# Optimization experiments

Measured on AMD Instinct MI355X. Metric: run time of the kernel, lower is better.

## Reference

```python
import jax, jax.numpy as jnp
import numpy as np

R = 6                 # max displacement / padding
D = 2 * R + 1         # window side; D*D = 169 displacements


def setup_inputs() -> dict:
    key = jax.random.key(0)
    k1, k2, k3 = jax.random.split(key, 3)
    b, cf, h, w = 2, 32, 256, 256
    feats_t = jax.random.normal(k1, (b, cf, h, w), jnp.float32)
    feats_r = jax.random.normal(k2, (b, cf, h, w), jnp.float32)
    img_r = jax.random.uniform(k3, (b, 1, h, w), jnp.float32)
    return {"feats_t": feats_t, "feats_r": feats_r, "img_r": img_r}


def _forward(feats_t, feats_r, img_r):
    b, cf, h, w = feats_t.shape
    ci = img_r.shape[1]
    x2p = jnp.pad(feats_r, ((0, 0), (0, 0), (R, R), (R, R)))
    imgp = jnp.pad(img_r, ((0, 0), (0, 0), (R, R), (R, R)))
    # displacement offsets in the same order as the torch double loop (_y outer, _x inner)
    offs = jnp.stack(
        jnp.meshgrid(jnp.arange(D), jnp.arange(D), indexing="ij"), axis=-1
    ).reshape(-1, 2)

    def step(carry, off):
        dy, dx = off[0], off[1]
        win = jax.lax.dynamic_slice(x2p, (0, 0, dy, dx), (b, cf, h, w))
        c = jnp.sum(feats_t * win, axis=1)  # [b, h, w] correlation for this displacement
        iw = jax.lax.dynamic_slice(imgp, (0, 0, dy, dx), (b, ci, h, w))
        return carry, (c, iw)

    _, (corr, imgs) = jax.lax.scan(step, 0, offs)  # corr: [D*D, b, h, w]; imgs: [D*D, b, ci, h, w]
    attn = jax.nn.softmax(corr, axis=0)  # softmax over displacements (torch dim=1 channel axis)
    # weighted sum of shifted reference images -> warped target image
    return jnp.einsum("dbhw,dbchw->bchw", attn, imgs)


def reference(feats_t, feats_r, img_r):
    return _forward(feats_t, feats_r, img_r)
```

## Files before the change

### kernel.cpp

```cpp
#include <hip/hip_runtime.h>
#include <stdint.h>

typedef _Float16 half_t;
typedef _Float16 v4h __attribute__((ext_vector_type(4)));
typedef _Float16 v8h __attribute__((ext_vector_type(8)));
typedef float v4f __attribute__((ext_vector_type(4)));

#define HH 256
#define WW 256
#define HW (HH*WW)
#define TH 32
#define TW 16
#define NROWS (TH+12)
#define NPX   (TW+16)
#define PXS   40
#define NTHREADS 1024
#define NUNITS (NROWS*64)
#define L2E 1.44269504088896340736f

__global__ __launch_bounds__(NTHREADS, 4)
void corr_recon(const float* __restrict__ ft, const float* __restrict__ fr,
                const float* __restrict__ img, float* __restrict__ out)
{
    __shared__ half_t frl[NROWS * NPX * PXS];
    __shared__ float  img_lds[NROWS * NPX];

    const int bid0 = blockIdx.x;
    const int bid  = (bid0 & 7) * 32 + (bid0 >> 3);

    const int b0  = bid >> 7;
    const int rb  = bid & 127;
    const int y0  = (rb >> 4) * TH;
    const int x0t = (rb & 15) * TW;

    const int tid  = threadIdx.x;
    const int lane = tid & 63;
    const int w    = tid >> 6;
    const int n    = lane & 15;
    const int g    = lane >> 4;

    const float* frb = fr  + (size_t)b0 * 32 * HW;
    const float* ftb = ft  + (size_t)b0 * 32 * HW;
    const float* imb = img + (size_t)b0 * HW;

    auto ld_unit = [&](int i, float4* t4) {
        const int px4 = i & 7;
        const int q   = (i >> 3) & 7;
        const int row = i >> 6;
        const int gy  = y0 - 6 + row;
        const int gx  = x0t - 6 + px4 * 4;
        const int gyc = min(max(gy, 0), HH-1);
        const bool oky = (gy == gyc);
        const float* src = frb + ((size_t)(4*q) * HH + gyc) * WW;
        if (oky && gx >= 0 && gx + 3 < WW) {
            #pragma unroll
            for (int jc = 0; jc < 4; ++jc)
                t4[jc] = *(const float4*)(src + (size_t)jc * HW + gx);
        } else {
            #pragma unroll
            for (int jc = 0; jc < 4; ++jc) {
                float e0 = 0.f, e1 = 0.f, e2 = 0.f, e3 = 0.f;
                const float* s = src + (size_t)jc * HW;
                if (oky) {
                    int x0 = gx, x1 = gx+1, x2 = gx+2, x3 = gx+3;
                    e0 = (x0 >= 0 && x0 < WW) ? s[x0] : 0.f;
                    e1 = (x1 >= 0 && x1 < WW) ? s[x1] : 0.f;
                    e2 = (x2 >= 0 && x2 < WW) ? s[x2] : 0.f;
                    e3 = (x3 >= 0 && x3 < WW) ? s[x3] : 0.f;
                }
                t4[jc].x = e0; t4[jc].y = e1; t4[jc].z = e2; t4[jc].w = e3;
            }
        }
    };
    auto wr_unit = [&](int i, const float4* t4) {
        const int px4 = i & 7;
        const int q   = (i >> 3) & 7;
        const int row = i >> 6;
        const int qo  = 8*(q & 3) + 4*(q >> 2);
        const float t0[4] = {t4[0].x, t4[0].y, t4[0].z, t4[0].w};
        const float t1[4] = {t4[1].x, t4[1].y, t4[1].z, t4[1].w};
        const float t2[4] = {t4[2].x, t4[2].y, t4[2].z, t4[2].w};
        const float t3[4] = {t4[3].x, t4[3].y, t4[3].z, t4[3].w};
        #pragma unroll
        for (int jp = 0; jp < 4; ++jp) {
            const int px = px4 * 4 + jp;
            v4h pk;
            pk[0] = (half_t)t0[jp]; pk[1] = (half_t)t1[jp];
            pk[2] = (half_t)t2[jp]; pk[3] = (half_t)t3[jp];
            *(v4h*)&frl[(row * NPX + px) * PXS + qo] = pk;
        }
    };

    {
        float4 tA[4], tB[4];
        ld_unit(tid, tA);
        ld_unit(tid + NTHREADS, tB);
        wr_unit(tid, tA);
        if (tid < NUNITS - 2*NTHREADS)
            ld_unit(tid + 2*NTHREADS, tA);
        wr_unit(tid + NTHREADS, tB);
        if (tid < NUNITS - 2*NTHREADS)
            wr_unit(tid + 2*NTHREADS, tA);
    }

    if (tid < NROWS * 8) {
        const int px4 = tid & 7;
        const int row = tid >> 3;
        const int gy = y0 - 6 + row;
        const int gx = x0t - 6 + px4*4;
        const int gyc = min(max(gy, 0), HH-1);
        const bool oky = (gy == gyc);
        const float* p = imb + (size_t)gyc * WW;
        float v[4];
        if (oky && gx >= 0 && gx + 3 < WW) {
            float4 t4 = *(const float4*)(p + gx);
            v[0]=t4.x; v[1]=t4.y; v[2]=t4.z; v[3]=t4.w;
        } else {
            #pragma unroll
            for (int e = 0; e < 4; ++e) {
                int x = gx + e;
                v[e] = (oky && x >= 0 && x < WW) ? p[x] : 0.f;
            }
        }
        float4 f4; f4.x=v[0]; f4.y=v[1]; f4.z=v[2]; f4.w=v[3];
        *(float4*)&img_lds[row*NPX + px4*4] = f4;
    }

    const int y = y0 + 2*w;
    v8h a0, a1;
    {
        const float* fa = ftb + (size_t)y * WW + (x0t + n);
        #pragma unroll
        for (int j = 0; j < 4; ++j) {
            a0[j]   = (half_t)(fa[(size_t)(4*g + j)      * HW] * L2E);
            a0[4+j] = (half_t)(fa[(size_t)(16 + 4*g + j) * HW] * L2E);
            a1[j]   = (half_t)(fa[WW + (size_t)(4*g + j)      * HW] * L2E);
            a1[4+j] = (half_t)(fa[WW + (size_t)(16 + 4*g + j) * HW] * L2E);
        }
    }

    v4f bias0, bias1;
    #pragma unroll
    for (int r = 0; r < 4; ++r) {
        const int m  = 4*g + r;
        const int d0 = n - m;
        const int d1 = 16 + n - m;
        bias0[r] = (d0 >= 0 && d0 <= 12) ? 0.f : -1e4f;
        bias1[r] = (d1 >= 0 && d1 <= 12) ? 0.f : -1e4f;
    }
    const int dm = n - 4*g;

    __syncthreads();

    v4f lp0 = {0,0,0,0}, ap0 = {0,0,0,0};
    v4f lp1 = {0,0,0,0}, ap1 = {0,0,0,0};

    auto STEP = [&](const v8h& a, v4f& lp, v4f& ap,
                    const v8h& B0, const v8h& B1, float iw0, float iw1) {
        v4f c0 = __builtin_amdgcn_mfma_f32_16x16x32_f16(a, B0, bias0, 0, 0, 0);
        v4f c1 = __builtin_amdgcn_mfma_f32_16x16x32_f16(a, B1, bias1, 0, 0, 0);
        #pragma unroll
        for (int r = 0; r < 4; ++r) {
            const bool cond = (dm >= r);
            float cs  = cond ? c0[r] : c1[r];
            float iws = cond ? iw0   : iw1;
            float e = __builtin_amdgcn_exp2f(cs);
            lp[r] += e;
            ap[r] += e * iws;
        }
    };

    const half_t* prd = &frl[(2*w * NPX + n) * PXS + 8*g];
    const float*  ird = &img_lds[2*w * NPX + n];

    v8h C0 = *(const v8h*)(prd);
    v8h C1 = *(const v8h*)(prd + 16*PXS);
    float ci0 = ird[0], ci1 = ird[16];

    prd += NPX*PXS; ird += NPX;
    v8h N0 = *(const v8h*)(prd);
    v8h N1 = *(const v8h*)(prd + 16*PXS);
    float ni0 = ird[0], ni1 = ird[16];

    STEP(a0, lp0, ap0, C0, C1, ci0, ci1);

    #pragma unroll 1
    for (int rr = 1; rr < 13; ++rr) {
        C0 = N0; C1 = N1; ci0 = ni0; ci1 = ni1;
        prd += NPX*PXS; ird += NPX;
        N0 = *(const v8h*)(prd);
        N1 = *(const v8h*)(prd + 16*PXS);
        ni0 = ird[0]; ni1 = ird[16];
        STEP(a0, lp0, ap0, C0, C1, ci0, ci1);
        STEP(a1, lp1, ap1, C0, C1, ci0, ci1);
    }
    STEP(a1, lp1, ap1, N0, N1, ni0, ni1);

    #pragma unroll
    for (int r = 0; r < 4; ++r) {
        float l0 = lp0[r], v0 = ap0[r], l1 = lp1[r], v1 = ap1[r];
        l0 += __shfl_xor(l0, 1);  v0 += __shfl_xor(v0, 1);
        l1 += __shfl_xor(l1, 1);  v1 += __shfl_xor(v1, 1);
        l0 += __shfl_xor(l0, 2);  v0 += __shfl_xor(v0, 2);
        l1 += __shfl_xor(l1, 2);  v1 += __shfl_xor(v1, 2);
        l0 += __shfl_xor(l0, 4);  v0 += __shfl_xor(v0, 4);
        l1 += __shfl_xor(l1, 4);  v1 += __shfl_xor(v1, 4);
        l0 += __shfl_xor(l0, 8);  v0 += __shfl_xor(v0, 8);
        l1 += __shfl_xor(l1, 8);  v1 += __shfl_xor(v1, 8);
        lp0[r] = l0; ap0[r] = v0; lp1[r] = l1; ap1[r] = v1;
    }
    if (n < 4) {
        const float l0 = n==0 ? lp0[0] : n==1 ? lp0[1] : n==2 ? lp0[2] : lp0[3];
        const float v0 = n==0 ? ap0[0] : n==1 ? ap0[1] : n==2 ? ap0[2] : ap0[3];
        const float l1 = n==0 ? lp1[0] : n==1 ? lp1[1] : n==2 ? lp1[2] : lp1[3];
        const float v1 = n==0 ? ap1[0] : n==1 ? ap1[1] : n==2 ? ap1[2] : ap1[3];
        float* orow = out + (size_t)b0 * HW + (size_t)y * WW + x0t + 4*g + n;
        orow[0]  = v0 / l0;
        orow[WW] = v1 / l1;
    }
}

extern "C" void kernel_launch(void* const* d_in, const int* in_sizes, int n_in,
                              void* d_out, int out_size, void* d_ws, size_t ws_size,
                              hipStream_t stream)
{
    const float* ft  = (const float*)d_in[0];
    const float* fr  = (const float*)d_in[1];
    const float* img = (const float*)d_in[2];
    float* out = (float*)d_out;
    (void)in_sizes; (void)n_in; (void)out_size; (void)d_ws; (void)ws_size;
    corr_recon<<<256, NTHREADS, 0, stream>>>(ft, fr, img, out);
}
```

Baseline: 19.09 us.

## Stage LDS fill in three phases overlapped with partial per-warp compute

The single up-front fill of the shared reference-feature tile, followed by one barrier, is replaced by three phases of 16 rows each. After each phase, every warp processes as many displacement rows as are already in shared memory. Meanwhile the global loads for the next 16 rows are in flight and are written to shared memory afterwards. The aim is to hide global-load latency behind MFMA and exp work, at the cost of two extra block barriers and four extra padded rows of loads.

Result: slower. 20.97 us (+9.9%).

```diff
diff --git a/kernel.cpp b/kernel.cpp
--- a/kernel.cpp
+++ b/kernel.cpp
@@ -11,19 +11,18 @@
 #define HW (HH*WW)
 #define TH 32
 #define TW 16
-#define NROWS (TH+12)
+#define NRLDS 48
 #define NPX   (TW+16)
 #define PXS   40
 #define NTHREADS 1024
-#define NUNITS (NROWS*64)
 #define L2E 1.44269504088896340736f
 
 __global__ __launch_bounds__(NTHREADS, 4)
 void corr_recon(const float* __restrict__ ft, const float* __restrict__ fr,
                 const float* __restrict__ img, float* __restrict__ out)
 {
-    __shared__ half_t frl[NROWS * NPX * PXS];
-    __shared__ float  img_lds[NROWS * NPX];
+    __shared__ half_t frl[NRLDS * NPX * PXS];
+    __shared__ float  img_lds[NRLDS * NPX];
 
     const int bid0 = blockIdx.x;
     const int bid  = (bid0 & 7) * 32 + (bid0 >> 3);
@@ -43,7 +42,7 @@
     const float* ftb = ft  + (size_t)b0 * 32 * HW;
     const float* imb = img + (size_t)b0 * HW;
 
-    auto ld_unit = [&](int i, float4* t4) {
+    auto LD = [&](int i, float4* t4) {
         const int px4 = i & 7;
         const int q   = (i >> 3) & 7;
         const int row = i >> 6;
@@ -59,20 +58,19 @@
         } else {
             #pragma unroll
             for (int jc = 0; jc < 4; ++jc) {
-                float e0 = 0.f, e1 = 0.f, e2 = 0.f, e3 = 0.f;
                 const float* s = src + (size_t)jc * HW;
+                float e0=0.f, e1=0.f, e2=0.f, e3=0.f;
                 if (oky) {
-                    int x0 = gx, x1 = gx+1, x2 = gx+2, x3 = gx+3;
-                    e0 = (x0 >= 0 && x0 < WW) ? s[x0] : 0.f;
-                    e1 = (x1 >= 0 && x1 < WW) ? s[x1] : 0.f;
-                    e2 = (x2 >= 0 && x2 < WW) ? s[x2] : 0.f;
-                    e3 = (x3 >= 0 && x3 < WW) ? s[x3] : 0.f;
+                    e0 = (gx   >= 0 && gx   < WW) ? s[gx]   : 0.f;
+                    e1 = (gx+1 >= 0 && gx+1 < WW) ? s[gx+1] : 0.f;
+                    e2 = (gx+2 >= 0 && gx+2 < WW) ? s[gx+2] : 0.f;
+                    e3 = (gx+3 >= 0 && gx+3 < WW) ? s[gx+3] : 0.f;
                 }
-                t4[jc].x = e0; t4[jc].y = e1; t4[jc].z = e2; t4[jc].w = e3;
+                t4[jc].x=e0; t4[jc].y=e1; t4[jc].z=e2; t4[jc].w=e3;
             }
         }
     };
-    auto wr_unit = [&](int i, const float4* t4) {
+    auto WR = [&](int i, const float4* t4) {
         const int px4 = i & 7;
         const int q   = (i >> 3) & 7;
         const int row = i >> 6;
@@ -91,19 +89,10 @@
         }
     };
 
-    {
-        float4 tA[4], tB[4];
-        ld_unit(tid, tA);
-        ld_unit(tid + NTHREADS, tB);
-        wr_unit(tid, tA);
-        if (tid < NUNITS - 2*NTHREADS)
-            ld_unit(tid + 2*NTHREADS, tA);
-        wr_unit(tid + NTHREADS, tB);
-        if (tid < NUNITS - 2*NTHREADS)
-            wr_unit(tid + 2*NTHREADS, tA);
-    }
-
-    if (tid < NROWS * 8) {
+    float4 tc[4], tn[4];
+    LD(tid, tc);
+
+    if (tid < NRLDS * 8) {
         const int px4 = tid & 7;
         const int row = tid >> 3;
         const int gy = y0 - 6 + row;
@@ -139,6 +128,9 @@
         }
     }
 
+    WR(tid, tc);
+    LD(tid + NTHREADS, tn);
+
     v4f bias0, bias1;
     #pragma unroll
     for (int r = 0; r < 4; ++r) {
@@ -150,10 +142,13 @@
     }
     const int dm = n - 4*g;
 
-    __syncthreads();
-
     v4f lp0 = {0,0,0,0}, ap0 = {0,0,0,0};
     v4f lp1 = {0,0,0,0}, ap1 = {0,0,0,0};
+    const half_t* prd = &frl[(2*w * NPX + n) * PXS + 8*g];
+    const float*  ird = &img_lds[2*w * NPX + n];
+    v8h C0, C1, N0, N1;
+    float ci0 = 0.f, ci1 = 0.f, ni0 = 0.f, ni1 = 0.f;
+    int rr = 0;
 
     auto STEP = [&](const v8h& a, v4f& lp, v4f& ap,
                     const v8h& B0, const v8h& B1, float iw0, float iw1) {
@@ -170,31 +165,47 @@
         }
     };
 
-    const half_t* prd = &frl[(2*w * NPX + n) * PXS + 8*g];
-    const float*  ird = &img_lds[2*w * NPX + n];
-
-    v8h C0 = *(const v8h*)(prd);
-    v8h C1 = *(const v8h*)(prd + 16*PXS);
-    float ci0 = ird[0], ci1 = ird[16];
-
-    prd += NPX*PXS; ird += NPX;
-    v8h N0 = *(const v8h*)(prd);
-    v8h N1 = *(const v8h*)(prd + 16*PXS);
-    float ni0 = ird[0], ni1 = ird[16];
-
-    STEP(a0, lp0, ap0, C0, C1, ci0, ci1);
-
-    #pragma unroll 1
-    for (int rr = 1; rr < 13; ++rr) {
-        C0 = N0; C1 = N1; ci0 = ni0; ci1 = ni1;
-        prd += NPX*PXS; ird += NPX;
-        N0 = *(const v8h*)(prd);
-        N1 = *(const v8h*)(prd + 16*PXS);
-        ni0 = ird[0]; ni1 = ird[16];
-        STEP(a0, lp0, ap0, C0, C1, ci0, ci1);
-        STEP(a1, lp1, ap1, C0, C1, ci0, ci1);
-    }
-    STEP(a1, lp1, ap1, N0, N1, ni0, ni1);
+    auto run_until = [&](int lim) {
+        if (lim > 14) lim = 14;
+        if (rr >= lim) return;
+        if (rr == 0) {
+            C0 = *(const v8h*)(prd);  C1 = *(const v8h*)(prd + 16*PXS);
+            ci0 = ird[0]; ci1 = ird[16];
+            prd += NPX*PXS; ird += NPX;
+            N0 = *(const v8h*)(prd);  N1 = *(const v8h*)(prd + 16*PXS);
+            ni0 = ird[0]; ni1 = ird[16];
+            STEP(a0, lp0, ap0, C0, C1, ci0, ci1);
+            rr = 1;
+        }
+        const int top = (lim < 13) ? lim : 13;
+        #pragma unroll 1
+        for (; rr < top; ++rr) {
+            C0 = N0; C1 = N1; ci0 = ni0; ci1 = ni1;
+            prd += NPX*PXS; ird += NPX;
+            N0 = *(const v8h*)(prd);
+            N1 = *(const v8h*)(prd + 16*PXS);
+            ni0 = ird[0]; ni1 = ird[16];
+            STEP(a0, lp0, ap0, C0, C1, ci0, ci1);
+            STEP(a1, lp1, ap1, C0, C1, ci0, ci1);
+        }
+        if (lim == 14 && rr == 13) {
+            STEP(a1, lp1, ap1, N0, N1, ni0, ni1);
+            rr = 14;
+        }
+    };
+
+    __syncthreads();
+
+    run_until(15 - 2*w);
+    WR(tid + NTHREADS, tn);
+    LD(tid + 2*NTHREADS, tn);
+    __syncthreads();
+
+    run_until(31 - 2*w);
+    WR(tid + 2*NTHREADS, tn);
+    __syncthreads();
+
+    run_until(14);
 
     #pragma unroll
     for (int r = 0; r < 4; ++r) {
```

## Split LDS staging into two phases to overlap reference-feature loads with compute

Applied to the files above, without the earlier changes.

The reference-feature tile is now staged in two parts. The first 29 rows are written to LDS and the first half of the output rows is computed while the remaining rows are fetched from global memory. Those rows are written to LDS afterwards, behind a second barrier. Each wave now processes rows w and w+16 instead of two adjacent rows, which lets the first half depend only on the early rows. The cost is that the two row passes no longer share the B-fragment and image reads from LDS, so LDS read traffic doubles, and there is an extra barrier.

Result: slower. 21.09 us (+10.5%).

```diff
diff --git a/kernel.cpp b/kernel.cpp
--- a/kernel.cpp
+++ b/kernel.cpp
@@ -11,19 +11,20 @@
 #define HW (HH*WW)
 #define TH 32
 #define TW 16
-#define NROWS (TH+12)
+#define NRLDS 45
 #define NPX   (TW+16)
 #define PXS   40
+#define RSTEP (NPX*PXS)
 #define NTHREADS 1024
-#define NUNITS (NROWS*64)
+#define UA 1856
 #define L2E 1.44269504088896340736f
 
 __global__ __launch_bounds__(NTHREADS, 4)
 void corr_recon(const float* __restrict__ ft, const float* __restrict__ fr,
                 const float* __restrict__ img, float* __restrict__ out)
 {
-    __shared__ half_t frl[NROWS * NPX * PXS];
-    __shared__ float  img_lds[NROWS * NPX];
+    __shared__ half_t frl[NRLDS * RSTEP];
+    __shared__ float  img_lds[NRLDS * NPX];
 
     const int bid0 = blockIdx.x;
     const int bid  = (bid0 & 7) * 32 + (bid0 >> 3);
@@ -43,7 +44,7 @@
     const float* ftb = ft  + (size_t)b0 * 32 * HW;
     const float* imb = img + (size_t)b0 * HW;
 
-    auto ld_unit = [&](int i, float4* t4) {
+    auto LD = [&](int i, float4* t4) {
         const int px4 = i & 7;
         const int q   = (i >> 3) & 7;
         const int row = i >> 6;
@@ -59,20 +60,19 @@
         } else {
             #pragma unroll
             for (int jc = 0; jc < 4; ++jc) {
-                float e0 = 0.f, e1 = 0.f, e2 = 0.f, e3 = 0.f;
                 const float* s = src + (size_t)jc * HW;
+                float e0=0.f, e1=0.f, e2=0.f, e3=0.f;
                 if (oky) {
-                    int x0 = gx, x1 = gx+1, x2 = gx+2, x3 = gx+3;
-                    e0 = (x0 >= 0 && x0 < WW) ? s[x0] : 0.f;
-                    e1 = (x1 >= 0 && x1 < WW) ? s[x1] : 0.f;
-                    e2 = (x2 >= 0 && x2 < WW) ? s[x2] : 0.f;
-                    e3 = (x3 >= 0 && x3 < WW) ? s[x3] : 0.f;
+                    e0 = (gx   >= 0 && gx   < WW) ? s[gx]   : 0.f;
+                    e1 = (gx+1 >= 0 && gx+1 < WW) ? s[gx+1] : 0.f;
+                    e2 = (gx+2 >= 0 && gx+2 < WW) ? s[gx+2] : 0.f;
+                    e3 = (gx+3 >= 0 && gx+3 < WW) ? s[gx+3] : 0.f;
                 }
-                t4[jc].x = e0; t4[jc].y = e1; t4[jc].z = e2; t4[jc].w = e3;
+                t4[jc].x=e0; t4[jc].y=e1; t4[jc].z=e2; t4[jc].w=e3;
             }
         }
     };
-    auto wr_unit = [&](int i, const float4* t4) {
+    auto WR = [&](int i, const float4* t4) {
         const int px4 = i & 7;
         const int q   = (i >> 3) & 7;
         const int row = i >> 6;
@@ -91,19 +91,12 @@
         }
     };
 
-    {
-        float4 tA[4], tB[4];
-        ld_unit(tid, tA);
-        ld_unit(tid + NTHREADS, tB);
-        wr_unit(tid, tA);
-        if (tid < NUNITS - 2*NTHREADS)
-            ld_unit(tid + 2*NTHREADS, tA);
-        wr_unit(tid + NTHREADS, tB);
-        if (tid < NUNITS - 2*NTHREADS)
-            wr_unit(tid + 2*NTHREADS, tA);
-    }
-
-    if (tid < NROWS * 8) {
+    float4 tA[4], tB[4], tn[4];
+    LD(tid, tA);
+    const bool has2 = (tid < UA - NTHREADS);
+    if (has2) LD(tid + NTHREADS, tB);
+
+    if (tid < NRLDS * 8) {
         const int px4 = tid & 7;
         const int row = tid >> 3;
         const int gy = y0 - 6 + row;
@@ -126,7 +119,7 @@
         *(float4*)&img_lds[row*NPX + px4*4] = f4;
     }
 
-    const int y = y0 + 2*w;
+    const int y = y0 + w;
     v8h a0, a1;
     {
         const float* fa = ftb + (size_t)y * WW + (x0t + n);
@@ -134,10 +127,15 @@
         for (int j = 0; j < 4; ++j) {
             a0[j]   = (half_t)(fa[(size_t)(4*g + j)      * HW] * L2E);
             a0[4+j] = (half_t)(fa[(size_t)(16 + 4*g + j) * HW] * L2E);
-            a1[j]   = (half_t)(fa[WW + (size_t)(4*g + j)      * HW] * L2E);
-            a1[4+j] = (half_t)(fa[WW + (size_t)(16 + 4*g + j) * HW] * L2E);
-        }
-    }
+            a1[j]   = (half_t)(fa[16*WW + (size_t)(4*g + j)      * HW] * L2E);
+            a1[4+j] = (half_t)(fa[16*WW + (size_t)(16 + 4*g + j) * HW] * L2E);
+        }
+    }
+
+    WR(tid, tA);
+    if (has2) WR(tid + NTHREADS, tB);
+
+    LD(tid + UA, tn);
 
     v4f bias0, bias1;
     #pragma unroll
@@ -149,11 +147,6 @@
         bias1[r] = (d1 >= 0 && d1 <= 12) ? 0.f : -1e4f;
     }
     const int dm = n - 4*g;
-
-    __syncthreads();
-
-    v4f lp0 = {0,0,0,0}, ap0 = {0,0,0,0};
-    v4f lp1 = {0,0,0,0}, ap1 = {0,0,0,0};
 
     auto STEP = [&](const v8h& a, v4f& lp, v4f& ap,
                     const v8h& B0, const v8h& B1, float iw0, float iw1) {
@@ -170,31 +163,39 @@
         }
     };
 
-    const half_t* prd = &frl[(2*w * NPX + n) * PXS + 8*g];
-    const float*  ird = &img_lds[2*w * NPX + n];
-
-    v8h C0 = *(const v8h*)(prd);
-    v8h C1 = *(const v8h*)(prd + 16*PXS);
-    float ci0 = ird[0], ci1 = ird[16];
-
-    prd += NPX*PXS; ird += NPX;
-    v8h N0 = *(const v8h*)(prd);
-    v8h N1 = *(const v8h*)(prd + 16*PXS);
-    float ni0 = ird[0], ni1 = ird[16];
-
-    STEP(a0, lp0, ap0, C0, C1, ci0, ci1);
-
-    #pragma unroll 1
-    for (int rr = 1; rr < 13; ++rr) {
-        C0 = N0; C1 = N1; ci0 = ni0; ci1 = ni1;
-        prd += NPX*PXS; ird += NPX;
-        N0 = *(const v8h*)(prd);
-        N1 = *(const v8h*)(prd + 16*PXS);
-        ni0 = ird[0]; ni1 = ird[16];
-        STEP(a0, lp0, ap0, C0, C1, ci0, ci1);
-        STEP(a1, lp1, ap1, C0, C1, ci0, ci1);
-    }
-    STEP(a1, lp1, ap1, N0, N1, ni0, ni1);
+    auto half = [&](const v8h& a, int rowb, v4f& lp, v4f& ap) {
+        const half_t* prd = &frl[(rowb * NPX + n) * PXS + 8*g];
+        const float*  ird = &img_lds[rowb * NPX + n];
+        v8h C0 = *(const v8h*)(prd);
+        v8h C1 = *(const v8h*)(prd + 16*PXS);
+        float ci0 = ird[0], ci1 = ird[16];
+        prd += RSTEP; ird += NPX;
+        v8h N0 = *(const v8h*)(prd);
+        v8h N1 = *(const v8h*)(prd + 16*PXS);
+        float ni0 = ird[0], ni1 = ird[16];
+        STEP(a, lp, ap, C0, C1, ci0, ci1);
+        #pragma unroll 1
+        for (int rr = 1; rr < 13; ++rr) {
+            C0 = N0; C1 = N1; ci0 = ni0; ci1 = ni1;
+            prd += RSTEP; ird += NPX;
+            N0 = *(const v8h*)(prd);
+            N1 = *(const v8h*)(prd + 16*PXS);
+            ni0 = ird[0]; ni1 = ird[16];
+            STEP(a, lp, ap, C0, C1, ci0, ci1);
+        }
+    };
+
+    v4f lp0 = {0,0,0,0}, ap0 = {0,0,0,0};
+    v4f lp1 = {0,0,0,0}, ap1 = {0,0,0,0};
+
+    __syncthreads();
+
+    half(a0, w, lp0, ap0);
+
+    WR(tid + UA, tn);
+    __syncthreads();
+
+    half(a1, w + 16, lp1, ap1);
 
     #pragma unroll
     for (int r = 0; r < 4; ++r) {
@@ -214,9 +215,9 @@
         const float v0 = n==0 ? ap0[0] : n==1 ? ap0[1] : n==2 ? ap0[2] : ap0[3];
         const float l1 = n==0 ? lp1[0] : n==1 ? lp1[1] : n==2 ? lp1[2] : lp1[3];
         const float v1 = n==0 ? ap1[0] : n==1 ? ap1[1] : n==2 ? ap1[2] : ap1[3];
-        float* orow = out + (size_t)b0 * HW + (size_t)y * WW + x0t + 4*g + n;
-        orow[0]  = v0 / l0;
-        orow[WW] = v1 / l1;
+        float* op = out + (size_t)b0 * HW + (size_t)y * WW + x0t + 4*g + n;
+        op[0]       = v0 / l0;
+        op[16 * WW] = v1 / l1;
     }
 }
 
```
